# Optimization experiments

Measured on AMD Instinct MI355X. Metric: run time of the kernel, lower is better.

Reference implementation:

```python
import jax, jax.numpy as jnp
import numpy as np

B, F, H, N, S, L, E = 32, 128, 256, 2048, 3, 2, 262144
DEG = E // (B * N)  # average degree used to normalize position updates


def setup_inputs() -> dict:
    key = jax.random.key(0)
    ks = jax.random.split(key, 12)
    s = 0.05
    return {
        "x": jax.random.normal(ks[0], (B, F), jnp.float32),
        "positions": jax.random.normal(ks[1], (N, S), jnp.float32),
        "W_in": jax.random.normal(ks[2], (F, H), jnp.float32) * s,
        "b_in": jnp.zeros((H,), jnp.float32),
        "Wg1": jax.random.normal(ks[3], (3, H // 2), jnp.float32) * s,
        "bg1": jnp.zeros((H // 2,), jnp.float32),
        "Wg2": jax.random.normal(ks[4], (H // 2, H), jnp.float32) * s,
        "bg2": jnp.zeros((H,), jnp.float32),
        "Wm": jax.random.normal(ks[5], (L, 2 * H + 1, H), jnp.float32) * s,
        "bm": jnp.zeros((L, H), jnp.float32),
        "Wu": jax.random.normal(ks[6], (L, 2 * H, H), jnp.float32) * s,
        "bu": jnp.zeros((L, H), jnp.float32),
        "Wp": jax.random.normal(ks[7], (L, H, 1), jnp.float32) * s,
        "W_out": jax.random.normal(ks[8], (H, 1), jnp.float32) * s,
        "b_out": jnp.zeros((1,), jnp.float32),
        "edge_index": jax.random.randint(ks[9], (2, E), 0, B * N, dtype=jnp.int32),
    }


def _geometric_features(positions, Wg1, bg1, Wg2, bg2):
    # For single points, pairwise / centroid / Hausdorff distances all reduce to
    # the euclidean distance, so feature[i, 0..2] = mean_{j != i} ||p_i - p_j||.
    n = positions.shape[0]
    diff = positions[:, None, :] - positions[None, :, :]      # [N, N, S]
    dsq = jnp.sum(diff * diff, axis=-1)                        # [N, N]
    mask = 1.0 - jnp.eye(n, dtype=positions.dtype)
    d = jnp.sqrt(jnp.where(mask > 0, dsq, 1.0)) * mask         # grad-safe sqrt
    mean_d = jnp.sum(d, axis=1) / (n - 1)                      # [N]
    gf = jnp.stack([mean_d, mean_d, mean_d], axis=-1)          # [N, 3]
    return jax.nn.relu(gf @ Wg1 + bg1) @ Wg2 + bg2             # [N, H]


def _forward(x, positions, W_in, b_in, Wg1, bg1, Wg2, bg2, Wm, bm, Wu, bu, Wp, W_out, b_out, edge_index):
    nn_ = B * N
    h = x @ W_in + b_in                                        # [B, H]
    h = jnp.broadcast_to(h[:, None, :], (B, N, H)).reshape(nn_, H)
    pos = jnp.broadcast_to(positions[None], (B, N, S)).reshape(nn_, S)
    g = _geometric_features(positions, Wg1, bg1, Wg2, bg2)     # [N, H]
    h = h + jnp.broadcast_to(g[None], (B, N, H)).reshape(nn_, H)
    src, dst = edge_index[0], edge_index[1]
    for l in range(L):  # small fixed layer loop
        dvec = pos[src] - pos[dst]
        d = jnp.sqrt(jnp.sum(dvec * dvec, axis=-1, keepdims=True) + 1e-12)  # [E, 1]
        m = jax.nn.relu(jnp.concatenate([h[src], h[dst], d], axis=-1) @ Wm[l] + bm[l])
        agg = jax.ops.segment_sum(m, dst, num_segments=nn_)    # [B*N, H]
        coef = m @ Wp[l]                                       # [E, 1]
        pos = pos + jax.ops.segment_sum((pos[dst] - pos[src]) * coef, dst, num_segments=nn_) / DEG
        h = h + jax.nn.relu(jnp.concatenate([h, agg], axis=-1) @ Wu[l] + bu[l])
    out = (h.reshape(B, N, H) @ W_out + b_out).squeeze(-1)     # [B, N]
    return out


def reference(x, positions, W_in, b_in, Wg1, bg1, Wg2, bg2, Wm, bm, Wu, bu, Wp, W_out, b_out, edge_index):
    return _forward(x, positions, W_in, b_in, Wg1, bg1, Wg2, bg2, Wm, bm, Wu, bu, Wp, W_out, b_out, edge_index)
```

## Files before the change

kernel.cpp:

```cpp
#include <hip/hip_runtime.h>
#include <math.h>

#define B_ 32
#define F_ 128
#define H_ 256
#define N_ 2048
#define L_ 2
#define E_ 262144
#define NN_ 65536

typedef __attribute__((ext_vector_type(8))) short short8;
typedef __attribute__((ext_vector_type(4))) float f32x4;
typedef __attribute__((ext_vector_type(2))) float f32x2;

static __device__ __forceinline__ unsigned short f2bf(float f) {
  unsigned int u = __float_as_uint(f);
  u += 0x7FFF + ((u >> 16) & 1);
  return (unsigned short)(u >> 16);
}
static __device__ __forceinline__ float bf2f(unsigned short u) {
  return __uint_as_float(((unsigned int)u) << 16);
}
static __device__ __forceinline__ unsigned int pk_bf16(float lo, float hi) {
  unsigned int r;
  asm("v_cvt_pk_bf16_f32 %0, %1, %2" : "=v"(r) : "v"(lo), "v"(hi));
  return r;
}

typedef const __attribute__((address_space(1))) unsigned int* as1p;
typedef __attribute__((address_space(3))) unsigned int* as3p;
static __device__ __forceinline__ void gload16(const void* g, void* l) {
  __builtin_amdgcn_global_load_lds((as1p)g, (as3p)l, 16, 0, 0);
}


__global__ void h0_kernel(const float* __restrict__ x, const float* __restrict__ W_in,
                          const float* __restrict__ b_in, float* __restrict__ h0) {
  int b = blockIdx.x;
  int j = threadIdx.x;
  float acc = b_in[j];
#pragma unroll 8
  for (int k = 0; k < F_; ++k)
    acc += x[b * F_ + k] * W_in[k * H_ + j];
  h0[b * H_ + j] = acc;
}

__global__ void meand_g_kernel(const float* __restrict__ positions,
                               const float* __restrict__ Wg1, const float* __restrict__ bg1,
                               const float* __restrict__ Wg2, const float* __restrict__ bg2,
                               float* __restrict__ g) {
  __shared__ float red[256];
  __shared__ float hid[128];
  int n = blockIdx.x;
  int t = threadIdx.x;
  float px = positions[n * 3 + 0], py = positions[n * 3 + 1], pz = positions[n * 3 + 2];
  float s = 0.f;
  for (int j = t; j < N_; j += 256) {
    float dx = px - positions[j * 3 + 0];
    float dy = py - positions[j * 3 + 1];
    float dz = pz - positions[j * 3 + 2];
    s += sqrtf(dx * dx + dy * dy + dz * dz);
  }
  red[t] = s;
  __syncthreads();
  for (int off = 128; off > 0; off >>= 1) {
    if (t < off) red[t] += red[t + off];
    __syncthreads();
  }
  float md = red[0] / (float)(N_ - 1);
  if (t < 128) {
    float w = Wg1[t] + Wg1[128 + t] + Wg1[256 + t];
    hid[t] = fmaxf(md * w + bg1[t], 0.f);
  }
  __syncthreads();
  float acc = bg2[t];
#pragma unroll 8
  for (int k = 0; k < 128; ++k)
    acc += hid[k] * Wg2[k * H_ + t];
  g[n * H_ + t] = acc;
}

__global__ void hbfinit_kernel(const float* __restrict__ h0, const float* __restrict__ g,
                               unsigned short* __restrict__ hbf) {
  int idx = blockIdx.x * blockDim.x + threadIdx.x;
  int row = idx >> 5;
  int c8 = (idx & 31) << 3;
  const float* hp = h0 + (row >> 11) * H_ + c8;
  const float* gp = g + (row & (N_ - 1)) * H_ + c8;
  const float4 a = *(const float4*)hp;
  const float4 a2 = *(const float4*)(hp + 4);
  const float4 b = *(const float4*)gp;
  const float4 b2 = *(const float4*)(gp + 4);
  short8 v;
  v[0] = (short)f2bf(a.x + b.x);  v[1] = (short)f2bf(a.y + b.y);
  v[2] = (short)f2bf(a.z + b.z);  v[3] = (short)f2bf(a.w + b.w);
  v[4] = (short)f2bf(a2.x + b2.x); v[5] = (short)f2bf(a2.y + b2.y);
  v[6] = (short)f2bf(a2.z + b2.z); v[7] = (short)f2bf(a2.w + b2.w);
  *(short8*)(hbf + (((size_t)row) << 8) + c8) = v;
}

__global__ void hginit_kernel(const float* __restrict__ h0, const float* __restrict__ g,
                              unsigned short* __restrict__ hg) {
  int idx = blockIdx.x * blockDim.x + threadIdx.x;
  int row = idx >> 5;
  int c8 = (idx & 31) << 3;
  const float* src = (row < 2048) ? (g + (size_t)row * H_ + c8)
                                  : (h0 + (size_t)(row - 2048) * H_ + c8);
  const float4 a = *(const float4*)src;
  const float4 a2 = *(const float4*)(src + 4);
  short8 v;
  v[0] = (short)f2bf(a.x);  v[1] = (short)f2bf(a.y);
  v[2] = (short)f2bf(a.z);  v[3] = (short)f2bf(a.w);
  v[4] = (short)f2bf(a2.x); v[5] = (short)f2bf(a2.y);
  v[6] = (short)f2bf(a2.z); v[7] = (short)f2bf(a2.w);
  *(short8*)(hg + (((size_t)row) << 8) + c8) = v;
}

__global__ void posinit_kernel(const float* __restrict__ positions, float* __restrict__ pos4) {
  int n = blockIdx.x * blockDim.x + threadIdx.x;
  int src = (n & (N_ - 1)) * 3;
  float4 v;
  v.x = positions[src + 0];
  v.y = positions[src + 1];
  v.z = positions[src + 2];
  v.w = 0.f;
  *(float4*)(pos4 + ((size_t)n << 2)) = v;
}


__global__ void deg_kernel(const int* __restrict__ ei, int* __restrict__ deg) {
  int e = blockIdx.x * 256 + threadIdx.x;
  atomicAdd(&deg[ei[E_ + e]], 1);
}

__global__ void scan1_kernel(const int* __restrict__ deg, int* __restrict__ bsum) {
  __shared__ int red[256];
  int t = threadIdx.x;
  red[t] = deg[blockIdx.x * 256 + t];
  __syncthreads();
  for (int off = 128; off > 0; off >>= 1) {
    if (t < off) red[t] += red[t + off];
    __syncthreads();
  }
  if (t == 0) bsum[blockIdx.x] = red[0];
}

__global__ void scan2_kernel(int* __restrict__ bsum) {
  __shared__ int s[256];
  int t = threadIdx.x;
  s[t] = bsum[t];
  __syncthreads();
  for (int off = 1; off < 256; off <<= 1) {
    int v = (t >= off) ? s[t - off] : 0;
    __syncthreads();
    s[t] += v;
    __syncthreads();
  }
  bsum[t] = (t == 0) ? 0 : s[t - 1];
}

__global__ void scan3_kernel(const int* __restrict__ deg, const int* __restrict__ bsum,
                             int* __restrict__ cur, int* __restrict__ rowptr) {
  __shared__ int s[256];
  int t = threadIdx.x;
  int i = blockIdx.x * 256 + t;
  s[t] = deg[i];
  __syncthreads();
  for (int off = 1; off < 256; off <<= 1) {
    int v = (t >= off) ? s[t - off] : 0;
    __syncthreads();
    s[t] += v;
    __syncthreads();
  }
  int excl = (t == 0) ? 0 : s[t - 1];
  int v = bsum[blockIdx.x] + excl;
  cur[i] = v;
  rowptr[i] = v;
}

__global__ void scatter_kernel(const int* __restrict__ ei, int* __restrict__ cur,
                               int* __restrict__ src_s) {
  int e = blockIdx.x * 256 + threadIdx.x;
  int s = ei[e], d = ei[E_ + e];
  int p = atomicAdd(&cur[d], 1);
  src_s[p] = s;
}

__global__ void wconv_all(const float* __restrict__ Wm, const float* __restrict__ Wu,
                          unsigned short* __restrict__ Wt1, unsigned short* __restrict__ Wut) {
  int idx = blockIdx.x * 256 + threadIdx.x;
  int sel = idx >> 14;
  int rem = idx & 16383;
  if (sel < 2) {
    const float* W = Wm + (size_t)sel * 513 * H_;
    unsigned short* dst = Wt1 + (size_t)sel * 131072 + ((size_t)rem << 3);
    int g = rem >> 13;
    int r2 = rem & 8191;
    int kc = r2 >> 11, w = (r2 >> 9) & 3, ks = (r2 >> 8) & 1, ni = (r2 >> 6) & 3, lane = r2 & 63;
    int r = lane & 15, q = lane >> 4;
    int n  = (w << 6) + (ni << 4) + r;
    int kb = (g << 8) + (kc << 6) + (ks << 5) + (q << 3);
#pragma unroll
    for (int j = 0; j < 8; ++j)
      dst[j] = f2bf(W[(size_t)(kb + j) * H_ + n]);
  } else {
    const float* W = Wu + (size_t)(sel - 2) * 512 * H_;
    unsigned short* dst = Wut + (size_t)(sel - 2) * 131072 + ((size_t)rem << 3);
    int kc = rem >> 11, w = (rem >> 9) & 3, ks = (rem >> 8) & 1, ni = (rem >> 6) & 3, lane = rem & 63;
    int r = lane & 15, q = lane >> 4;
    int n  = (w << 6) + (ni << 4) + r;
    int kb = (kc << 6) + (ks << 5) + (q << 3);
#pragma unroll
    for (int j = 0; j < 8; ++j)
      dst[j] = f2bf(W[(size_t)(kb + j) * H_ + n]);
  }
}


#define GEMM_IDS                                                     \
  const int t = threadIdx.x;                                         \
  const int m0 = blockIdx.x << 6;                                    \
  const int wu = __builtin_amdgcn_readfirstlane(t >> 6);             \
  const int lane = t & 63;                                           \
  const int q = lane >> 4;                                           \
  const int r = lane & 15;                                           \
  const int arow = lane >> 2;                                        \
  const int aq = (lane & 3) ^ ((lane >> 2) & 3);

#define STAGE_P(P, abase)                                                                \
  do {                                                                                   \
    gload16((abase) + (((size_t)(m0 + (wu << 4) + arow)) << 8) + (((P) & 7) << 5) +      \
                (aq << 3),                                                               \
            &sA[(P) & 3][wu << 9]);                                                      \
    _Pragma("unroll")                                                                    \
    for (int j_ = 0; j_ < 4; ++j_)                                                       \
      gload16(Wt + (((size_t)((P) >> 1)) << 14) + (wu << 12) + (((P) & 1) << 11) +       \
                  (j_ << 9) + (lane << 3),                                               \
              &sB[(P) & 3][(wu << 11) + (j_ << 9)]);                                     \
  } while (0)

#define COMPUTE_P(P)                                                                     \
  do {                                                                                   \
    short8 af[4], bfr[4];                                                                \
    _Pragma("unroll")                                                                    \
    for (int mi = 0; mi < 4; ++mi)                                                       \
      af[mi] = *(const short8*)(&sA[(P) & 3][((mi * 16 + r) << 5) +                      \
                                             ((q ^ (r & 3)) << 3)]);                     \
    _Pragma("unroll")                                                                    \
    for (int ni = 0; ni < 4; ++ni)                                                       \
      bfr[ni] = *(const short8*)(&sB[(P) & 3][(wu << 11) + (ni << 9) + (lane << 3)]);    \
    _Pragma("unroll")                                                                    \
    for (int mi = 0; mi < 4; ++mi)                                                       \
      _Pragma("unroll")                                                                  \
      for (int ni = 0; ni < 4; ++ni)                                                     \
        acc[mi][ni] = __builtin_amdgcn_mfma_f32_16x16x32_bf16(af[mi], bfr[ni],           \
                                                              acc[mi][ni], 0, 0, 0);     \
  } while (0)

#define WAIT_BAR(P)                                                       \
  do {                                                                    \
    if ((P) <= 13)      asm volatile("s_waitcnt vmcnt(10)" ::: "memory"); \
    else if ((P) == 14) asm volatile("s_waitcnt vmcnt(5)" ::: "memory");  \
    else                asm volatile("s_waitcnt vmcnt(0)" ::: "memory");  \
    __builtin_amdgcn_s_barrier();                                         \
    asm volatile("" ::: "memory");                                        \
  } while (0)

#define ACC_ZERO()                                   \
  _Pragma("unroll")                                  \
  for (int mi = 0; mi < 4; ++mi)                     \
    _Pragma("unroll")                                \
    for (int ni = 0; ni < 4; ++ni)                   \
      acc[mi][ni] = (f32x4){0.f, 0.f, 0.f, 0.f};

__launch_bounds__(256)
__global__ void gemm1_mfma(const unsigned short* __restrict__ hbf,
                           const unsigned short* __restrict__ Wt,
                           const float* __restrict__ bm,
                           unsigned short* __restrict__ X, unsigned short* __restrict__ Zb) {
  __shared__ __align__(16) unsigned short sA[4][2048];
  __shared__ __align__(16) unsigned short sB[4][8192];
  GEMM_IDS

  f32x4 acc[4][4];
  ACC_ZERO();

  STAGE_P(0, hbf); STAGE_P(1, hbf); STAGE_P(2, hbf);
#pragma unroll
  for (int p = 0; p < 16; ++p) {
    WAIT_BAR(p);
    if (p + 3 < 16) STAGE_P(p + 3, hbf);
    COMPUTE_P(p);
    if (p == 7) {
#pragma unroll
      for (int ni = 0; ni < 4; ++ni) {
        int n = (wu << 6) + ni * 16 + r;
#pragma unroll
        for (int mi = 0; mi < 4; ++mi)
#pragma unroll
          for (int reg = 0; reg < 4; ++reg) {
            size_t idx = (((size_t)(m0 + mi * 16 + q * 4 + reg)) << 8) + n;
            X[idx] = f2bf(acc[mi][ni][reg]);
            acc[mi][ni][reg] = 0.f;
          }
      }
    }
  }

#pragma unroll
  for (int ni = 0; ni < 4; ++ni) {
    int n = (wu << 6) + ni * 16 + r;
    float bmn = bm[n];
#pragma unroll
    for (int mi = 0; mi < 4; ++mi)
#pragma unroll
      for (int reg = 0; reg < 4; ++reg) {
        size_t idx = (((size_t)(m0 + mi * 16 + q * 4 + reg)) << 8) + n;
        Zb[idx] = f2bf(acc[mi][ni][reg] + bmn);
      }
  }
}

__launch_bounds__(256)
__global__ void gemm1_small(const unsigned short* __restrict__ hg,
                            const unsigned short* __restrict__ Wt,
                            const float* __restrict__ bm,
                            float* __restrict__ Xc, float* __restrict__ Zc) {
  __shared__ __align__(16) unsigned short sA[4][2048];
  __shared__ __align__(16) unsigned short sB[4][8192];
  GEMM_IDS

  f32x4 acc[4][4];
  ACC_ZERO();

  STAGE_P(0, hg); STAGE_P(1, hg); STAGE_P(2, hg);
#pragma unroll
  for (int p = 0; p < 16; ++p) {
    WAIT_BAR(p);
    if (p + 3 < 16) STAGE_P(p + 3, hg);
    COMPUTE_P(p);
    if (p == 7) {
#pragma unroll
      for (int ni = 0; ni < 4; ++ni) {
        int n = (wu << 6) + ni * 16 + r;
#pragma unroll
        for (int mi = 0; mi < 4; ++mi)
#pragma unroll
          for (int reg = 0; reg < 4; ++reg) {
            size_t idx = (((size_t)(m0 + mi * 16 + q * 4 + reg)) << 8) + n;
            Xc[idx] = acc[mi][ni][reg];
            acc[mi][ni][reg] = 0.f;
          }
      }
    }
  }

  const int isH0 = (blockIdx.x == 32);
#pragma unroll
  for (int ni = 0; ni < 4; ++ni) {
    int n = (wu << 6) + ni * 16 + r;
    float bmn = isH0 ? bm[n] : 0.f;
#pragma unroll
    for (int mi = 0; mi < 4; ++mi)
#pragma unroll
      for (int reg = 0; reg < 4; ++reg) {
        size_t idx = (((size_t)(m0 + mi * 16 + q * 4 + reg)) << 8) + n;
        Zc[idx] = acc[mi][ni][reg] + bmn;
      }
  }
}

static __device__ __forceinline__ void edge_core(
    const float4 pn, const float4 q,
    f32x2 x01, f32x2 x23,
    const f32x2 z01, const f32x2 z23,
    const f32x2 wl01, const f32x2 wl23,
    const f32x2 wp01, const f32x2 wp23,
    f32x2& a01, f32x2& a23,
    float& pdx, float& pdy, float& pdz) {
  const float dx = pn.x - q.x, dy = pn.y - q.y, dz = pn.z - q.z;
  const float d = sqrtf(dx * dx + dy * dy + dz * dz + 1e-12f);
  f32x2 dd; dd[0] = d; dd[1] = d;
  f32x2 v01 = x01 + z01 + dd * wl01;
  f32x2 v23 = x23 + z23 + dd * wl23;
  v01[0] = fmaxf(v01[0], 0.f); v01[1] = fmaxf(v01[1], 0.f);
  v23[0] = fmaxf(v23[0], 0.f); v23[1] = fmaxf(v23[1], 0.f);
  a01 += v01; a23 += v23;
  const f32x2 cpv = v01 * wp01 + v23 * wp23;
  const float cp = cpv[0] + cpv[1];
  pdx += dx * cp; pdy += dy * cp; pdz += dz * cp;
}

static __device__ __forceinline__ void edge_do(
    const float4 pn, const float4 q, const uint2 xv,
    const f32x2 z01, const f32x2 z23,
    const f32x2 wl01, const f32x2 wl23,
    const f32x2 wp01, const f32x2 wp23,
    f32x2& a01, f32x2& a23,
    float& pdx, float& pdy, float& pdz) {
  f32x2 x01, x23;
  x01[0] = __uint_as_float(xv.x << 16);
  x01[1] = __uint_as_float(xv.x & 0xffff0000u);
  x23[0] = __uint_as_float(xv.y << 16);
  x23[1] = __uint_as_float(xv.y & 0xffff0000u);
  edge_core(pn, q, x01, x23, z01, z23, wl01, wl23, wp01, wp23, a01, a23, pdx, pdy, pdz);
}

static __device__ __forceinline__ void edge_do0(
    const float4 pn, const float4 q, const float4 xg, const float4 xh,
    const f32x2 z01, const f32x2 z23,
    const f32x2 wl01, const f32x2 wl23,
    const f32x2 wp01, const f32x2 wp23,
    f32x2& a01, f32x2& a23,
    float& pdx, float& pdy, float& pdz) {
  f32x2 x01, x23;
  x01[0] = xg.x + xh.x; x01[1] = xg.y + xh.y;
  x23[0] = xg.z + xh.z; x23[1] = xg.w + xh.w;
  edge_core(pn, q, x01, x23, z01, z23, wl01, wl23, wp01, wp23, a01, a23, pdx, pdy, pdz);
}

__launch_bounds__(256)
__global__ void edge_kernel(const unsigned short* __restrict__ X,
                            const unsigned short* __restrict__ Zb,
                            const float* __restrict__ pos_c,
                            const int* __restrict__ rowptr, const int* __restrict__ src_s,
                            const float* __restrict__ wl, const float* __restrict__ wp,
                            unsigned short* __restrict__ aggb, float* __restrict__ pos_o) {
  const int gid = blockIdx.x * 256 + threadIdx.x;
  const int n = __builtin_amdgcn_readfirstlane(gid >> 6);
  const int lane = threadIdx.x & 63;

  const float4 wlv = *(const float4*)(wl + (lane << 2));
  const float4 wpv = *(const float4*)(wp + (lane << 2));
  const f32x2 wl01 = {wlv.x, wlv.y}, wl23 = {wlv.z, wlv.w};
  const f32x2 wp01 = {wpv.x, wpv.y}, wp23 = {wpv.z, wpv.w};

  const int e0 = rowptr[n];
  const int e1 = (n == NN_ - 1) ? E_ : rowptr[n + 1];

  const uint2 zv = *(const uint2*)(Zb + (((size_t)n) << 8) + (lane << 2));
  f32x2 z01, z23;
  z01[0] = __uint_as_float(zv.x << 16);
  z01[1] = __uint_as_float(zv.x & 0xffff0000u);
  z23[0] = __uint_as_float(zv.y << 16);
  z23[1] = __uint_as_float(zv.y & 0xffff0000u);

  const float4 pn = *(const float4*)(pos_c + ((size_t)n << 2));
  f32x2 a01 = {0.f, 0.f}, a23 = {0.f, 0.f};
  float pdx = 0.f, pdy = 0.f, pdz = 0.f;

  const unsigned short* Xl = X + (lane << 2);

  int e = e0;
  for (; e + 4 <= e1; e += 4) {
    const int s0 = src_s[e], s1 = src_s[e + 1], s2 = src_s[e + 2], s3 = src_s[e + 3];
    const float4 q0 = *(const float4*)(pos_c + ((size_t)s0 << 2));
    const float4 q1 = *(const float4*)(pos_c + ((size_t)s1 << 2));
    const float4 q2 = *(const float4*)(pos_c + ((size_t)s2 << 2));
    const float4 q3 = *(const float4*)(pos_c + ((size_t)s3 << 2));
    const uint2 x0 = *(const uint2*)(Xl + (((size_t)s0) << 8));
    const uint2 x1 = *(const uint2*)(Xl + (((size_t)s1) << 8));
    const uint2 x2 = *(const uint2*)(Xl + (((size_t)s2) << 8));
    const uint2 x3 = *(const uint2*)(Xl + (((size_t)s3) << 8));
    edge_do(pn, q0, x0, z01, z23, wl01, wl23, wp01, wp23, a01, a23, pdx, pdy, pdz);
    edge_do(pn, q1, x1, z01, z23, wl01, wl23, wp01, wp23, a01, a23, pdx, pdy, pdz);
    edge_do(pn, q2, x2, z01, z23, wl01, wl23, wp01, wp23, a01, a23, pdx, pdy, pdz);
    edge_do(pn, q3, x3, z01, z23, wl01, wl23, wp01, wp23, a01, a23, pdx, pdy, pdz);
  }
  if (e + 2 <= e1) {
    const int s0 = src_s[e], s1 = src_s[e + 1];
    const float4 q0 = *(const float4*)(pos_c + ((size_t)s0 << 2));
    const float4 q1 = *(const float4*)(pos_c + ((size_t)s1 << 2));
    const uint2 x0 = *(const uint2*)(Xl + (((size_t)s0) << 8));
    const uint2 x1 = *(const uint2*)(Xl + (((size_t)s1) << 8));
    edge_do(pn, q0, x0, z01, z23, wl01, wl23, wp01, wp23, a01, a23, pdx, pdy, pdz);
    edge_do(pn, q1, x1, z01, z23, wl01, wl23, wp01, wp23, a01, a23, pdx, pdy, pdz);
    e += 2;
  }
  if (e < e1) {
    const int s0 = src_s[e];
    const float4 q0 = *(const float4*)(pos_c + ((size_t)s0 << 2));
    const uint2 x0 = *(const uint2*)(Xl + (((size_t)s0) << 8));
    edge_do(pn, q0, x0, z01, z23, wl01, wl23, wp01, wp23, a01, a23, pdx, pdy, pdz);
  }

  uint2 av;
  av.x = pk_bf16(a01[0], a01[1]);
  av.y = pk_bf16(a23[0], a23[1]);
  *(uint2*)(aggb + (((size_t)n) << 8) + (lane << 2)) = av;

#pragma unroll
  for (int m = 1; m < 64; m <<= 1) {
    pdx += __shfl_xor(pdx, m, 64);
    pdy += __shfl_xor(pdy, m, 64);
    pdz += __shfl_xor(pdz, m, 64);
  }
  if (lane == 0) {
    float4 po;
    po.x = pn.x + pdx * 0.25f;
    po.y = pn.y + pdy * 0.25f;
    po.z = pn.z + pdz * 0.25f;
    po.w = 0.f;
    *(float4*)(pos_o + ((size_t)n << 2)) = po;
  }
}

__launch_bounds__(256)
__global__ void edge0_kernel(const float* __restrict__ Xc,
                             const float* __restrict__ Zc,
                             const float* __restrict__ pos_c,
                             const int* __restrict__ rowptr, const int* __restrict__ src_s,
                             const float* __restrict__ wl, const float* __restrict__ wp,
                             unsigned short* __restrict__ aggb, float* __restrict__ pos_o) {
  const int gid = blockIdx.x * 256 + threadIdx.x;
  const int n = __builtin_amdgcn_readfirstlane(gid >> 6);
  const int lane = threadIdx.x & 63;

  const float4 wlv = *(const float4*)(wl + (lane << 2));
  const float4 wpv = *(const float4*)(wp + (lane << 2));
  const f32x2 wl01 = {wlv.x, wlv.y}, wl23 = {wlv.z, wlv.w};
  const f32x2 wp01 = {wpv.x, wpv.y}, wp23 = {wpv.z, wpv.w};

  const int e0 = rowptr[n];
  const int e1 = (n == NN_ - 1) ? E_ : rowptr[n + 1];

  const float* Xl = Xc + (lane << 2);
  const float* Zl = Zc + (lane << 2);

  const float4 zg = *(const float4*)(Zl + (((size_t)(n & (N_ - 1))) << 8));
  const float4 zh = *(const float4*)(Zl + (((size_t)(2048 + (n >> 11))) << 8));
  f32x2 z01, z23;
  z01[0] = zg.x + zh.x; z01[1] = zg.y + zh.y;
  z23[0] = zg.z + zh.z; z23[1] = zg.w + zh.w;

  const float4 pn = *(const float4*)(pos_c + ((size_t)n << 2));
  f32x2 a01 = {0.f, 0.f}, a23 = {0.f, 0.f};
  float pdx = 0.f, pdy = 0.f, pdz = 0.f;

  int e = e0;
  for (; e + 4 <= e1; e += 4) {
    const int s0 = src_s[e], s1 = src_s[e + 1], s2 = src_s[e + 2], s3 = src_s[e + 3];
    const float4 q0 = *(const float4*)(pos_c + ((size_t)s0 << 2));
    const float4 q1 = *(const float4*)(pos_c + ((size_t)s1 << 2));
    const float4 q2 = *(const float4*)(pos_c + ((size_t)s2 << 2));
    const float4 q3 = *(const float4*)(pos_c + ((size_t)s3 << 2));
    const float4 xg0 = *(const float4*)(Xl + (((size_t)(s0 & (N_ - 1))) << 8));
    const float4 xh0 = *(const float4*)(Xl + (((size_t)(2048 + (s0 >> 11))) << 8));
    const float4 xg1 = *(const float4*)(Xl + (((size_t)(s1 & (N_ - 1))) << 8));
    const float4 xh1 = *(const float4*)(Xl + (((size_t)(2048 + (s1 >> 11))) << 8));
    const float4 xg2 = *(const float4*)(Xl + (((size_t)(s2 & (N_ - 1))) << 8));
    const float4 xh2 = *(const float4*)(Xl + (((size_t)(2048 + (s2 >> 11))) << 8));
    const float4 xg3 = *(const float4*)(Xl + (((size_t)(s3 & (N_ - 1))) << 8));
    const float4 xh3 = *(const float4*)(Xl + (((size_t)(2048 + (s3 >> 11))) << 8));
    edge_do0(pn, q0, xg0, xh0, z01, z23, wl01, wl23, wp01, wp23, a01, a23, pdx, pdy, pdz);
    edge_do0(pn, q1, xg1, xh1, z01, z23, wl01, wl23, wp01, wp23, a01, a23, pdx, pdy, pdz);
    edge_do0(pn, q2, xg2, xh2, z01, z23, wl01, wl23, wp01, wp23, a01, a23, pdx, pdy, pdz);
    edge_do0(pn, q3, xg3, xh3, z01, z23, wl01, wl23, wp01, wp23, a01, a23, pdx, pdy, pdz);
  }
  for (; e < e1; ++e) {
    const int s0 = src_s[e];
    const float4 q0 = *(const float4*)(pos_c + ((size_t)s0 << 2));
    const float4 xg0 = *(const float4*)(Xl + (((size_t)(s0 & (N_ - 1))) << 8));
    const float4 xh0 = *(const float4*)(Xl + (((size_t)(2048 + (s0 >> 11))) << 8));
    edge_do0(pn, q0, xg0, xh0, z01, z23, wl01, wl23, wp01, wp23, a01, a23, pdx, pdy, pdz);
  }

  uint2 av;
  av.x = pk_bf16(a01[0], a01[1]);
  av.y = pk_bf16(a23[0], a23[1]);
  *(uint2*)(aggb + (((size_t)n) << 8) + (lane << 2)) = av;

#pragma unroll
  for (int m = 1; m < 64; m <<= 1) {
    pdx += __shfl_xor(pdx, m, 64);
    pdy += __shfl_xor(pdy, m, 64);
    pdz += __shfl_xor(pdz, m, 64);
  }
  if (lane == 0) {
    float4 po;
    po.x = pn.x + pdx * 0.25f;
    po.y = pn.y + pdy * 0.25f;
    po.z = pn.z + pdz * 0.25f;
    po.w = 0.f;
    *(float4*)(pos_o + ((size_t)n << 2)) = po;
  }
}

__launch_bounds__(256)
__global__ void upd2_mfma(unsigned short* __restrict__ hbf,
                          const unsigned short* __restrict__ aggb,
                          const unsigned short* __restrict__ Wt,
                          const float* __restrict__ bu) {
  __shared__ __align__(16) unsigned short sA[4][2048];
  __shared__ __align__(16) unsigned short sB[4][8192];
  GEMM_IDS

  f32x4 acc[4][4];
  ACC_ZERO();

  const unsigned short* hb = (const unsigned short*)hbf;
  STAGE_P(0, hb); STAGE_P(1, hb); STAGE_P(2, hb);
#pragma unroll
  for (int p = 0; p < 16; ++p) {
    WAIT_BAR(p);
    if (p + 3 < 16) {
      const unsigned short* ab = (p + 3 < 8) ? hb : aggb;
      STAGE_P(p + 3, ab);
    }
    COMPUTE_P(p);
  }

#pragma unroll
  for (int ni = 0; ni < 4; ++ni) {
    int n = (wu << 6) + ni * 16 + r;
    float buv = bu[n];
#pragma unroll
    for (int mi = 0; mi < 4; ++mi)
#pragma unroll
      for (int reg = 0; reg < 4; ++reg) {
        size_t idx = (((size_t)(m0 + mi * 16 + q * 4 + reg)) << 8) + n;
        float v = bf2f(hbf[idx]) + fmaxf(acc[mi][ni][reg] + buv, 0.f);
        hbf[idx] = f2bf(v);
      }
  }
}

__launch_bounds__(256)
__global__ void upd2_out(const unsigned short* __restrict__ hbf,
                         const unsigned short* __restrict__ aggb,
                         const unsigned short* __restrict__ Wt,
                         const float* __restrict__ bu,
                         const float* __restrict__ Wout, const float* __restrict__ bout,
                         float* __restrict__ out) {
  __shared__ __align__(16) unsigned short sA[4][2048];
  __shared__ __align__(16) unsigned short sB[4][8192];
  GEMM_IDS

  f32x4 acc[4][4];
  ACC_ZERO();

  STAGE_P(0, hbf); STAGE_P(1, hbf); STAGE_P(2, hbf);
#pragma unroll
  for (int p = 0; p < 16; ++p) {
    WAIT_BAR(p);
    if (p + 3 < 16) {
      const unsigned short* ab = (p + 3 < 8) ? hbf : aggb;
      STAGE_P(p + 3, ab);
    }
    COMPUTE_P(p);
  }
  __syncthreads();
  float (*sRed)[64] = (float(*)[64])(&sA[0][0]);

  float dotp[4][4];
#pragma unroll
  for (int mi = 0; mi < 4; ++mi)
#pragma unroll
    for (int reg = 0; reg < 4; ++reg)
      dotp[mi][reg] = 0.f;

#pragma unroll
  for (int ni = 0; ni < 4; ++ni) {
    int n = (wu << 6) + ni * 16 + r;
    float buv = bu[n];
    float won = Wout[n];
#pragma unroll
    for (int mi = 0; mi < 4; ++mi)
#pragma unroll
      for (int reg = 0; reg < 4; ++reg) {
        size_t idx = (((size_t)(m0 + mi * 16 + q * 4 + reg)) << 8) + n;
        float v = bf2f(hbf[idx]) + fmaxf(acc[mi][ni][reg] + buv, 0.f);
        dotp[mi][reg] += v * won;
      }
  }
#pragma unroll
  for (int mask = 1; mask < 16; mask <<= 1)
#pragma unroll
    for (int mi = 0; mi < 4; ++mi)
#pragma unroll
      for (int reg = 0; reg < 4; ++reg)
        dotp[mi][reg] += __shfl_xor(dotp[mi][reg], mask, 64);
  if (r == 0) {
#pragma unroll
    for (int mi = 0; mi < 4; ++mi)
#pragma unroll
      for (int reg = 0; reg < 4; ++reg)
        sRed[wu][mi * 16 + q * 4 + reg] = dotp[mi][reg];
  }
  __syncthreads();
  if (t < 64)
    out[m0 + t] = sRed[0][t] + sRed[1][t] + sRed[2][t] + sRed[3][t] + bout[0];
}


extern "C" void kernel_launch(void* const* d_in, const int* in_sizes, int n_in,
                              void* d_out, int out_size, void* d_ws, size_t ws_size,
                              hipStream_t stream) {
  const float* x         = (const float*)d_in[0];
  const float* positions = (const float*)d_in[1];
  const float* W_in      = (const float*)d_in[2];
  const float* b_in      = (const float*)d_in[3];
  const float* Wg1       = (const float*)d_in[4];
  const float* bg1       = (const float*)d_in[5];
  const float* Wg2       = (const float*)d_in[6];
  const float* bg2       = (const float*)d_in[7];
  const float* Wm        = (const float*)d_in[8];
  const float* bm        = (const float*)d_in[9];
  const float* Wu        = (const float*)d_in[10];
  const float* bu        = (const float*)d_in[11];
  const float* Wp        = (const float*)d_in[12];
  const float* W_out     = (const float*)d_in[13];
  const float* b_out     = (const float*)d_in[14];
  const int*   ei        = (const int*)d_in[15];
  float* out = (float*)d_out;

  char* ws = (char*)d_ws;
  unsigned short* hbf   = (unsigned short*)(ws);
  unsigned short* X     = (unsigned short*)(ws +  33554432UL);
  unsigned short* Zb    = (unsigned short*)(ws +  67108864UL);
  unsigned short* aggb  = (unsigned short*)(ws + 100663296UL);
  float*          posA  = (float*)(ws + 134217728UL);
  float*          posB  = (float*)(ws + 135266304UL);
  float*          g     = (float*)(ws + 136314880UL);
  float*          h0    = (float*)(ws + 138412032UL);
  unsigned short* Wt1   = (unsigned short*)(ws + 138444800UL);
  unsigned short* Wut   = (unsigned short*)(ws + 138969088UL);
  int*            deg   = (int*)(ws + 139493376UL);
  int*            cur   = (int*)(ws + 139755520UL);
  int*            bsum  = (int*)(ws + 140017664UL);
  int*            rowptr= (int*)(ws + 140018688UL);
  int*            src_s = (int*)(ws + 140280832UL);

  unsigned short* hg = aggb;
  float*          Xc = (float*)X;
  float*          Zc = (float*)Zb;

  hipMemsetAsync(deg, 0, (size_t)NN_ * sizeof(int), stream);
  deg_kernel<<<E_ / 256, 256, 0, stream>>>(ei, deg);
  scan1_kernel<<<256, 256, 0, stream>>>(deg, bsum);
  scan2_kernel<<<1, 256, 0, stream>>>(bsum);
  scan3_kernel<<<256, 256, 0, stream>>>(deg, bsum, cur, rowptr);
  scatter_kernel<<<E_ / 256, 256, 0, stream>>>(ei, cur, src_s);

  wconv_all<<<256, 256, 0, stream>>>(Wm, Wu, Wt1, Wut);

  h0_kernel<<<B_, 256, 0, stream>>>(x, W_in, b_in, h0);
  meand_g_kernel<<<N_, 256, 0, stream>>>(positions, Wg1, bg1, Wg2, bg2, g);
  hbfinit_kernel<<<NN_ * 32 / 256, 256, 0, stream>>>(h0, g, hbf);
  hginit_kernel<<<2080 * 32 / 256, 256, 0, stream>>>(h0, g, hg);
  posinit_kernel<<<NN_ / 256, 256, 0, stream>>>(positions, posA);

  gemm1_small<<<33, 256, 0, stream>>>(hg, Wt1, bm, Xc, Zc);
  edge0_kernel<<<NN_ / 4, 256, 0, stream>>>(Xc, Zc, posA, rowptr, src_s,
                                            Wm + 512 * H_, Wp, aggb, posB);
  upd2_mfma<<<NN_ / 64, 256, 0, stream>>>(hbf, aggb, Wut, bu);

  gemm1_mfma<<<NN_ / 64, 256, 0, stream>>>(hbf, Wt1 + 131072,
                                           bm + H_, X, Zb);
  edge_kernel<<<NN_ / 4, 256, 0, stream>>>(X, Zb, posB, rowptr, src_s,
                                           Wm + (size_t)513 * H_ + 512 * H_,
                                           Wp + H_, aggb, posA);
  upd2_out<<<NN_ / 64, 256, 0, stream>>>(hbf, aggb, Wut + 131072,
                                         bu + H_, W_out, b_out, out);
}
```

Before: 324.5 us.

## Process two nodes per wavefront in edge kernels with 8-channel lanes

Both edge kernels now map each half-wavefront (32 lanes) to one destination node, with each lane handling 8 channels instead of 4, so a 64-lane wave covers two nodes and the grid is halved. Per-edge gathers become 16-byte (bf16) or two float4 loads per lane, and the edge loop becomes a masked two-edge step that runs until both half-waves finish. Node degree can differ between the two halves, so the wave runs for the larger degree and masked lanes do dummy loads. Register pressure per lane rises, and the unroll drops from four edges to two.

New measurement: 341.3 us. 1.05x slower.

```diff
diff --git a/kernel.cpp b/kernel.cpp
--- a/kernel.cpp
+++ b/kernel.cpp
@@ -370,53 +370,39 @@
   }
 }
 
-static __device__ __forceinline__ void edge_core(
-    const float4 pn, const float4 q,
-    f32x2 x01, f32x2 x23,
-    const f32x2 z01, const f32x2 z23,
-    const f32x2 wl01, const f32x2 wl23,
-    const f32x2 wp01, const f32x2 wp23,
-    f32x2& a01, f32x2& a23,
-    float& pdx, float& pdy, float& pdz) {
-  const float dx = pn.x - q.x, dy = pn.y - q.y, dz = pn.z - q.z;
-  const float d = sqrtf(dx * dx + dy * dy + dz * dz + 1e-12f);
+static __device__ __forceinline__ void edge_ch8(
+    float dx, float dy, float dz, float d, float vm,
+    const f32x2* xx, const f32x2* zz,
+    const f32x2* wl8, const f32x2* wp8,
+    f32x2* aa, float& pdx, float& pdy, float& pdz) {
   f32x2 dd; dd[0] = d; dd[1] = d;
-  f32x2 v01 = x01 + z01 + dd * wl01;
-  f32x2 v23 = x23 + z23 + dd * wl23;
-  v01[0] = fmaxf(v01[0], 0.f); v01[1] = fmaxf(v01[1], 0.f);
-  v23[0] = fmaxf(v23[0], 0.f); v23[1] = fmaxf(v23[1], 0.f);
-  a01 += v01; a23 += v23;
-  const f32x2 cpv = v01 * wp01 + v23 * wp23;
+  f32x2 vv; vv[0] = vm; vv[1] = vm;
+  f32x2 cpv = {0.f, 0.f};
+#pragma unroll
+  for (int i = 0; i < 4; ++i) {
+    f32x2 v = xx[i] + zz[i] + dd * wl8[i];
+    v[0] = fmaxf(v[0], 0.f); v[1] = fmaxf(v[1], 0.f);
+    v = v * vv;
+    aa[i] += v;
+    cpv += v * wp8[i];
+  }
   const float cp = cpv[0] + cpv[1];
   pdx += dx * cp; pdy += dy * cp; pdz += dz * cp;
 }
 
-static __device__ __forceinline__ void edge_do(
-    const float4 pn, const float4 q, const uint2 xv,
-    const f32x2 z01, const f32x2 z23,
-    const f32x2 wl01, const f32x2 wl23,
-    const f32x2 wp01, const f32x2 wp23,
-    f32x2& a01, f32x2& a23,
-    float& pdx, float& pdy, float& pdz) {
-  f32x2 x01, x23;
-  x01[0] = __uint_as_float(xv.x << 16);
-  x01[1] = __uint_as_float(xv.x & 0xffff0000u);
-  x23[0] = __uint_as_float(xv.y << 16);
-  x23[1] = __uint_as_float(xv.y & 0xffff0000u);
-  edge_core(pn, q, x01, x23, z01, z23, wl01, wl23, wp01, wp23, a01, a23, pdx, pdy, pdz);
-}
-
-static __device__ __forceinline__ void edge_do0(
-    const float4 pn, const float4 q, const float4 xg, const float4 xh,
-    const f32x2 z01, const f32x2 z23,
-    const f32x2 wl01, const f32x2 wl23,
-    const f32x2 wp01, const f32x2 wp23,
-    f32x2& a01, f32x2& a23,
-    float& pdx, float& pdy, float& pdz) {
-  f32x2 x01, x23;
-  x01[0] = xg.x + xh.x; x01[1] = xg.y + xh.y;
-  x23[0] = xg.z + xh.z; x23[1] = xg.w + xh.w;
-  edge_core(pn, q, x01, x23, z01, z23, wl01, wl23, wp01, wp23, a01, a23, pdx, pdy, pdz);
+static __device__ __forceinline__ void load8f(const float* p, f32x2* o) {
+  const float4 a = *(const float4*)p;
+  const float4 b = *(const float4*)(p + 4);
+  o[0][0] = a.x; o[0][1] = a.y;
+  o[1][0] = a.z; o[1][1] = a.w;
+  o[2][0] = b.x; o[2][1] = b.y;
+  o[3][0] = b.z; o[3][1] = b.w;
+}
+static __device__ __forceinline__ void unpack8(const uint4 u, f32x2* o) {
+  o[0][0] = __uint_as_float(u.x << 16); o[0][1] = __uint_as_float(u.x & 0xffff0000u);
+  o[1][0] = __uint_as_float(u.y << 16); o[1][1] = __uint_as_float(u.y & 0xffff0000u);
+  o[2][0] = __uint_as_float(u.z << 16); o[2][1] = __uint_as_float(u.z & 0xffff0000u);
+  o[3][0] = __uint_as_float(u.w << 16); o[3][1] = __uint_as_float(u.w & 0xffff0000u);
 }
 
 __launch_bounds__(256)
@@ -427,75 +413,72 @@
                             const float* __restrict__ wl, const float* __restrict__ wp,
                             unsigned short* __restrict__ aggb, float* __restrict__ pos_o) {
   const int gid = blockIdx.x * 256 + threadIdx.x;
-  const int n = __builtin_amdgcn_readfirstlane(gid >> 6);
+  const int wid = gid >> 6;
   const int lane = threadIdx.x & 63;
-
-  const float4 wlv = *(const float4*)(wl + (lane << 2));
-  const float4 wpv = *(const float4*)(wp + (lane << 2));
-  const f32x2 wl01 = {wlv.x, wlv.y}, wl23 = {wlv.z, wlv.w};
-  const f32x2 wp01 = {wpv.x, wpv.y}, wp23 = {wpv.z, wpv.w};
-
-  const int e0 = rowptr[n];
-  const int e1 = (n == NN_ - 1) ? E_ : rowptr[n + 1];
-
-  const uint2 zv = *(const uint2*)(Zb + (((size_t)n) << 8) + (lane << 2));
-  f32x2 z01, z23;
-  z01[0] = __uint_as_float(zv.x << 16);
-  z01[1] = __uint_as_float(zv.x & 0xffff0000u);
-  z23[0] = __uint_as_float(zv.y << 16);
-  z23[1] = __uint_as_float(zv.y & 0xffff0000u);
+  const int half = lane >> 5;
+  const int sl = lane & 31;
+  const int n = (wid << 1) + half;
+  const int c0 = sl << 3;
+
+  f32x2 wl8[4], wp8[4];
+  load8f(wl + c0, wl8);
+  load8f(wp + c0, wp8);
+
+  f32x2 z8[4];
+  unpack8(*(const uint4*)(Zb + (((size_t)n) << 8) + c0), z8);
 
   const float4 pn = *(const float4*)(pos_c + ((size_t)n << 2));
-  f32x2 a01 = {0.f, 0.f}, a23 = {0.f, 0.f};
+
+  int me = rowptr[n];
+  const int mend = (n == NN_ - 1) ? E_ : rowptr[n + 1];
+
+  f32x2 aa[4] = {{0.f,0.f},{0.f,0.f},{0.f,0.f},{0.f,0.f}};
   float pdx = 0.f, pdy = 0.f, pdz = 0.f;
 
-  const unsigned short* Xl = X + (lane << 2);
-
-  int e = e0;
-  for (; e + 4 <= e1; e += 4) {
-    const int s0 = src_s[e], s1 = src_s[e + 1], s2 = src_s[e + 2], s3 = src_s[e + 3];
+  const unsigned short* Xl = X + c0;
+
+  while (__any(me < mend)) {
+    const bool a0 = me < mend;
+    const bool a1 = (me + 1) < mend;
+    const int ce0 = a0 ? me : 0;
+    const int ce1 = a1 ? (me + 1) : 0;
+    const float vm0 = a0 ? 1.f : 0.f;
+    const float vm1 = a1 ? 1.f : 0.f;
+    const int s0 = src_s[ce0];
+    const int s1 = src_s[ce1];
     const float4 q0 = *(const float4*)(pos_c + ((size_t)s0 << 2));
     const float4 q1 = *(const float4*)(pos_c + ((size_t)s1 << 2));
-    const float4 q2 = *(const float4*)(pos_c + ((size_t)s2 << 2));
-    const float4 q3 = *(const float4*)(pos_c + ((size_t)s3 << 2));
-    const uint2 x0 = *(const uint2*)(Xl + (((size_t)s0) << 8));
-    const uint2 x1 = *(const uint2*)(Xl + (((size_t)s1) << 8));
-    const uint2 x2 = *(const uint2*)(Xl + (((size_t)s2) << 8));
-    const uint2 x3 = *(const uint2*)(Xl + (((size_t)s3) << 8));
-    edge_do(pn, q0, x0, z01, z23, wl01, wl23, wp01, wp23, a01, a23, pdx, pdy, pdz);
-    edge_do(pn, q1, x1, z01, z23, wl01, wl23, wp01, wp23, a01, a23, pdx, pdy, pdz);
-    edge_do(pn, q2, x2, z01, z23, wl01, wl23, wp01, wp23, a01, a23, pdx, pdy, pdz);
-    edge_do(pn, q3, x3, z01, z23, wl01, wl23, wp01, wp23, a01, a23, pdx, pdy, pdz);
-  }
-  if (e + 2 <= e1) {
-    const int s0 = src_s[e], s1 = src_s[e + 1];
-    const float4 q0 = *(const float4*)(pos_c + ((size_t)s0 << 2));
-    const float4 q1 = *(const float4*)(pos_c + ((size_t)s1 << 2));
-    const uint2 x0 = *(const uint2*)(Xl + (((size_t)s0) << 8));
-    const uint2 x1 = *(const uint2*)(Xl + (((size_t)s1) << 8));
-    edge_do(pn, q0, x0, z01, z23, wl01, wl23, wp01, wp23, a01, a23, pdx, pdy, pdz);
-    edge_do(pn, q1, x1, z01, z23, wl01, wl23, wp01, wp23, a01, a23, pdx, pdy, pdz);
-    e += 2;
-  }
-  if (e < e1) {
-    const int s0 = src_s[e];
-    const float4 q0 = *(const float4*)(pos_c + ((size_t)s0 << 2));
-    const uint2 x0 = *(const uint2*)(Xl + (((size_t)s0) << 8));
-    edge_do(pn, q0, x0, z01, z23, wl01, wl23, wp01, wp23, a01, a23, pdx, pdy, pdz);
-  }
-
-  uint2 av;
-  av.x = pk_bf16(a01[0], a01[1]);
-  av.y = pk_bf16(a23[0], a23[1]);
-  *(uint2*)(aggb + (((size_t)n) << 8) + (lane << 2)) = av;
-
-#pragma unroll
-  for (int m = 1; m < 64; m <<= 1) {
+    const uint4 u0 = *(const uint4*)(Xl + (((size_t)s0) << 8));
+    const uint4 u1 = *(const uint4*)(Xl + (((size_t)s1) << 8));
+    {
+      f32x2 x8[4]; unpack8(u0, x8);
+      const float dx = pn.x - q0.x, dy = pn.y - q0.y, dz = pn.z - q0.z;
+      const float d = sqrtf(dx * dx + dy * dy + dz * dz + 1e-12f);
+      edge_ch8(dx, dy, dz, d, vm0, x8, z8, wl8, wp8, aa, pdx, pdy, pdz);
+    }
+    {
+      f32x2 x8[4]; unpack8(u1, x8);
+      const float dx = pn.x - q1.x, dy = pn.y - q1.y, dz = pn.z - q1.z;
+      const float d = sqrtf(dx * dx + dy * dy + dz * dz + 1e-12f);
+      edge_ch8(dx, dy, dz, d, vm1, x8, z8, wl8, wp8, aa, pdx, pdy, pdz);
+    }
+    me += 2;
+  }
+
+  uint4 av;
+  av.x = pk_bf16(aa[0][0], aa[0][1]);
+  av.y = pk_bf16(aa[1][0], aa[1][1]);
+  av.z = pk_bf16(aa[2][0], aa[2][1]);
+  av.w = pk_bf16(aa[3][0], aa[3][1]);
+  *(uint4*)(aggb + (((size_t)n) << 8) + c0) = av;
+
+#pragma unroll
+  for (int m = 1; m < 32; m <<= 1) {
     pdx += __shfl_xor(pdx, m, 64);
     pdy += __shfl_xor(pdy, m, 64);
     pdz += __shfl_xor(pdz, m, 64);
   }
-  if (lane == 0) {
+  if (sl == 0) {
     float4 po;
     po.x = pn.x + pdx * 0.25f;
     po.y = pn.y + pdy * 0.25f;
@@ -513,70 +496,85 @@
                              const float* __restrict__ wl, const float* __restrict__ wp,
                              unsigned short* __restrict__ aggb, float* __restrict__ pos_o) {
   const int gid = blockIdx.x * 256 + threadIdx.x;
-  const int n = __builtin_amdgcn_readfirstlane(gid >> 6);
+  const int wid = gid >> 6;
   const int lane = threadIdx.x & 63;
-
-  const float4 wlv = *(const float4*)(wl + (lane << 2));
-  const float4 wpv = *(const float4*)(wp + (lane << 2));
-  const f32x2 wl01 = {wlv.x, wlv.y}, wl23 = {wlv.z, wlv.w};
-  const f32x2 wp01 = {wpv.x, wpv.y}, wp23 = {wpv.z, wpv.w};
-
-  const int e0 = rowptr[n];
-  const int e1 = (n == NN_ - 1) ? E_ : rowptr[n + 1];
-
-  const float* Xl = Xc + (lane << 2);
-  const float* Zl = Zc + (lane << 2);
-
-  const float4 zg = *(const float4*)(Zl + (((size_t)(n & (N_ - 1))) << 8));
-  const float4 zh = *(const float4*)(Zl + (((size_t)(2048 + (n >> 11))) << 8));
-  f32x2 z01, z23;
-  z01[0] = zg.x + zh.x; z01[1] = zg.y + zh.y;
-  z23[0] = zg.z + zh.z; z23[1] = zg.w + zh.w;
+  const int half = lane >> 5;
+  const int sl = lane & 31;
+  const int n = (wid << 1) + half;
+  const int c0 = sl << 3;
+
+  f32x2 wl8[4], wp8[4];
+  load8f(wl + c0, wl8);
+  load8f(wp + c0, wp8);
+
+  const float* Xl = Xc + c0;
+  const float* Zl = Zc + c0;
+
+  f32x2 z8[4];
+  {
+    f32x2 zg[4], zh[4];
+    load8f(Zl + (((size_t)(n & (N_ - 1))) << 8), zg);
+    load8f(Zl + (((size_t)(2048 + (n >> 11))) << 8), zh);
+#pragma unroll
+    for (int i = 0; i < 4; ++i) z8[i] = zg[i] + zh[i];
+  }
 
   const float4 pn = *(const float4*)(pos_c + ((size_t)n << 2));
-  f32x2 a01 = {0.f, 0.f}, a23 = {0.f, 0.f};
+
+  int me = rowptr[n];
+  const int mend = (n == NN_ - 1) ? E_ : rowptr[n + 1];
+
+  f32x2 aa[4] = {{0.f,0.f},{0.f,0.f},{0.f,0.f},{0.f,0.f}};
   float pdx = 0.f, pdy = 0.f, pdz = 0.f;
 
-  int e = e0;
-  for (; e + 4 <= e1; e += 4) {
-    const int s0 = src_s[e], s1 = src_s[e + 1], s2 = src_s[e + 2], s3 = src_s[e + 3];
+  while (__any(me < mend)) {
+    const bool a0 = me < mend;
+    const bool a1 = (me + 1) < mend;
+    const int ce0 = a0 ? me : 0;
+    const int ce1 = a1 ? (me + 1) : 0;
+    const float vm0 = a0 ? 1.f : 0.f;
+    const float vm1 = a1 ? 1.f : 0.f;
+    const int s0 = src_s[ce0];
+    const int s1 = src_s[ce1];
     const float4 q0 = *(const float4*)(pos_c + ((size_t)s0 << 2));
     const float4 q1 = *(const float4*)(pos_c + ((size_t)s1 << 2));
-    const float4 q2 = *(const float4*)(pos_c + ((size_t)s2 << 2));
-    const float4 q3 = *(const float4*)(pos_c + ((size_t)s3 << 2));
-    const float4 xg0 = *(const float4*)(Xl + (((size_t)(s0 & (N_ - 1))) << 8));
-    const float4 xh0 = *(const float4*)(Xl + (((size_t)(2048 + (s0 >> 11))) << 8));
-    const float4 xg1 = *(const float4*)(Xl + (((size_t)(s1 & (N_ - 1))) << 8));
-    const float4 xh1 = *(const float4*)(Xl + (((size_t)(2048 + (s1 >> 11))) << 8));
-    const float4 xg2 = *(const float4*)(Xl + (((size_t)(s2 & (N_ - 1))) << 8));
-    const float4 xh2 = *(const float4*)(Xl + (((size_t)(2048 + (s2 >> 11))) << 8));
-    const float4 xg3 = *(const float4*)(Xl + (((size_t)(s3 & (N_ - 1))) << 8));
-    const float4 xh3 = *(const float4*)(Xl + (((size_t)(2048 + (s3 >> 11))) << 8));
-    edge_do0(pn, q0, xg0, xh0, z01, z23, wl01, wl23, wp01, wp23, a01, a23, pdx, pdy, pdz);
-    edge_do0(pn, q1, xg1, xh1, z01, z23, wl01, wl23, wp01, wp23, a01, a23, pdx, pdy, pdz);
-    edge_do0(pn, q2, xg2, xh2, z01, z23, wl01, wl23, wp01, wp23, a01, a23, pdx, pdy, pdz);
-    edge_do0(pn, q3, xg3, xh3, z01, z23, wl01, wl23, wp01, wp23, a01, a23, pdx, pdy, pdz);
-  }
-  for (; e < e1; ++e) {
-    const int s0 = src_s[e];
-    const float4 q0 = *(const float4*)(pos_c + ((size_t)s0 << 2));
-    const float4 xg0 = *(const float4*)(Xl + (((size_t)(s0 & (N_ - 1))) << 8));
-    const float4 xh0 = *(const float4*)(Xl + (((size_t)(2048 + (s0 >> 11))) << 8));
-    edge_do0(pn, q0, xg0, xh0, z01, z23, wl01, wl23, wp01, wp23, a01, a23, pdx, pdy, pdz);
-  }
-
-  uint2 av;
-  av.x = pk_bf16(a01[0], a01[1]);
-  av.y = pk_bf16(a23[0], a23[1]);
-  *(uint2*)(aggb + (((size_t)n) << 8) + (lane << 2)) = av;
-
-#pragma unroll
-  for (int m = 1; m < 64; m <<= 1) {
+    {
+      f32x2 xg[4], xh[4], x8[4];
+      load8f(Xl + (((size_t)(s0 & (N_ - 1))) << 8), xg);
+      load8f(Xl + (((size_t)(2048 + (s0 >> 11))) << 8), xh);
+#pragma unroll
+      for (int i = 0; i < 4; ++i) x8[i] = xg[i] + xh[i];
+      const float dx = pn.x - q0.x, dy = pn.y - q0.y, dz = pn.z - q0.z;
+      const float d = sqrtf(dx * dx + dy * dy + dz * dz + 1e-12f);
+      edge_ch8(dx, dy, dz, d, vm0, x8, z8, wl8, wp8, aa, pdx, pdy, pdz);
+    }
+    {
+      f32x2 xg[4], xh[4], x8[4];
+      load8f(Xl + (((size_t)(s1 & (N_ - 1))) << 8), xg);
+      load8f(Xl + (((size_t)(2048 + (s1 >> 11))) << 8), xh);
+#pragma unroll
+      for (int i = 0; i < 4; ++i) x8[i] = xg[i] + xh[i];
+      const float dx = pn.x - q1.x, dy = pn.y - q1.y, dz = pn.z - q1.z;
+      const float d = sqrtf(dx * dx + dy * dy + dz * dz + 1e-12f);
+      edge_ch8(dx, dy, dz, d, vm1, x8, z8, wl8, wp8, aa, pdx, pdy, pdz);
+    }
+    me += 2;
+  }
+
+  uint4 av;
+  av.x = pk_bf16(aa[0][0], aa[0][1]);
+  av.y = pk_bf16(aa[1][0], aa[1][1]);
+  av.z = pk_bf16(aa[2][0], aa[2][1]);
+  av.w = pk_bf16(aa[3][0], aa[3][1]);
+  *(uint4*)(aggb + (((size_t)n) << 8) + c0) = av;
+
+#pragma unroll
+  for (int m = 1; m < 32; m <<= 1) {
     pdx += __shfl_xor(pdx, m, 64);
     pdy += __shfl_xor(pdy, m, 64);
     pdz += __shfl_xor(pdz, m, 64);
   }
-  if (lane == 0) {
+  if (sl == 0) {
     float4 po;
     po.x = pn.x + pdx * 0.25f;
     po.y = pn.y + pdy * 0.25f;
@@ -751,13 +749,13 @@
   posinit_kernel<<<NN_ / 256, 256, 0, stream>>>(positions, posA);
 
   gemm1_small<<<33, 256, 0, stream>>>(hg, Wt1, bm, Xc, Zc);
-  edge0_kernel<<<NN_ / 4, 256, 0, stream>>>(Xc, Zc, posA, rowptr, src_s,
+  edge0_kernel<<<NN_ / 8, 256, 0, stream>>>(Xc, Zc, posA, rowptr, src_s,
                                             Wm + 512 * H_, Wp, aggb, posB);
   upd2_mfma<<<NN_ / 64, 256, 0, stream>>>(hbf, aggb, Wut, bu);
 
   gemm1_mfma<<<NN_ / 64, 256, 0, stream>>>(hbf, Wt1 + 131072,
                                            bm + H_, X, Zb);
-  edge_kernel<<<NN_ / 4, 256, 0, stream>>>(X, Zb, posB, rowptr, src_s,
+  edge_kernel<<<NN_ / 8, 256, 0, stream>>>(X, Zb, posB, rowptr, src_s,
                                            Wm + (size_t)513 * H_ + 512 * H_,
                                            Wp + H_, aggb, posA);
   upd2_out<<<NN_ / 64, 256, 0, stream>>>(hbf, aggb, Wut + 131072,
```
